# Kernel optimization log

Measured on AMD Instinct MI355X. Metric: run time of the kernel, lower is better.

Reference implementation:

```python
import jax, jax.numpy as jnp
import numpy as np
from jax import lax

IN_F = 512   # encoder output dim
MEL = 80     # mel bins (memory_dim)
R = 7        # reduction factor
ATT = 128    # attention dim
B = 64
T_ENC = 512
T_MEL = 700  # must be divisible by R -> 100 decoder steps


def _gru(x, h, w_ih, w_hh, b_ih, b_hh):
    # torch.nn.GRUCell math
    gi = x @ w_ih.T + b_ih
    gh = h @ w_hh.T + b_hh
    ir, iz, inn = jnp.split(gi, 3, axis=-1)
    hr, hz, hn = jnp.split(gh, 3, axis=-1)
    r = jax.nn.sigmoid(ir + hr)
    z = jax.nn.sigmoid(iz + hz)
    return (1.0 - z) * jnp.tanh(inn + r * hn) + z * h


_PARAM_SHAPES = {
    'prenet_w1': (256, MEL), 'prenet_b1': (256,),
    'prenet_w2': (128, 256), 'prenet_b2': (128,),
    'attrnn_w_ih': (768, IN_F + 128), 'attrnn_w_hh': (768, 256),
    'attrnn_b_ih': (768,), 'attrnn_b_hh': (768,),
    'q_w': (ATT, 256), 'inp_w': (ATT, IN_F), 'v_w': (1, ATT), 'v_b': (1,),
    'loc_conv': (32, 2, 31), 'loc_w': (ATT, 32),
    'pd_w': (256, 256 + IN_F), 'pd_b': (256,),
    'dec1_w_ih': (768, 256), 'dec1_w_hh': (768, 256), 'dec1_b_ih': (768,), 'dec1_b_hh': (768,),
    'dec2_w_ih': (768, 256), 'dec2_w_hh': (768, 256), 'dec2_b_ih': (768,), 'dec2_b_hh': (768,),
    'mel_w': (MEL * R, 256), 'mel_b': (MEL * R,),
    'stop_w': (1, 256 + MEL * R), 'stop_b': (1,),
}


def setup_inputs() -> dict:
    key = jax.random.key(0)
    ks = iter(jax.random.split(key, 40))
    d = {
        'inputs': jax.random.normal(next(ks), (B, T_ENC, IN_F), jnp.float32),
        'memory': jax.random.normal(next(ks), (B, T_MEL, MEL), jnp.float32),
        'mask': jnp.ones((B, T_ENC), dtype=bool),
    }
    for n, s in _PARAM_SHAPES.items():
        d[n] = jax.random.normal(next(ks), s, jnp.float32) * 0.02
    return d


def reference(inputs, memory, mask, prenet_w1, prenet_b1, prenet_w2, prenet_b2,
              attrnn_w_ih, attrnn_w_hh, attrnn_b_ih, attrnn_b_hh,
              q_w, inp_w, v_w, v_b, loc_conv, loc_w, pd_w, pd_b,
              dec1_w_ih, dec1_w_hh, dec1_b_ih, dec1_b_hh,
              dec2_w_ih, dec2_w_hh, dec2_b_ih, dec2_b_hh,
              mel_w, mel_b, stop_w, stop_b):
    Bq, T_enc, _ = inputs.shape
    # attention.preprocess_inputs: [B, T_enc, ATT], computed once
    proc_in = jnp.einsum('btd,ad->bta', inputs, inp_w)
    # _reshape_memory: [B, T_mel, MEL] -> [T_steps, B, R*MEL]
    mem = memory.reshape(Bq, -1, R * MEL).transpose(1, 0, 2)
    # teacher forcing: step 0 uses zero memory_input, step t uses frame t-1
    xs = jnp.concatenate([jnp.zeros_like(mem[:1]), mem[:-1]], axis=0)

    def step(carry, x):
        h_att, h1, h2, ctx, aw, awc = carry
        # memory_size<=0 path: keep last mel frame of previous group
        m_in = x[:, MEL * (R - 1):]
        # prenet (original, dropout disabled)
        p = jax.nn.relu(m_in @ prenet_w1.T + prenet_b1)
        p = jax.nn.relu(p @ prenet_w2.T + prenet_b2)
        # attention RNN
        h_att = _gru(jnp.concatenate([p, ctx], axis=-1), h_att,
                     attrnn_w_ih, attrnn_w_hh, attrnn_b_ih, attrnn_b_hh)
        # location-sensitive attention
        pq = h_att @ q_w.T                              # [B, ATT]
        loc = jnp.stack([aw, awc], axis=1)              # [B, 2, T_enc]
        pl = lax.conv_general_dilated(loc, loc_conv, (1,), [(15, 15)],
                                      dimension_numbers=('NCH', 'OIH', 'NCH'))
        pl = jnp.einsum('bct,ac->bta', pl, loc_w)       # [B, T_enc, ATT]
        e = (jnp.tanh(pq[:, None, :] + proc_in + pl) @ v_w.T)[..., 0] + v_b
        e = jnp.where(mask, e, -1e9)
        align = jax.nn.softmax(e, axis=-1)              # [B, T_enc]
        ctx = jnp.einsum('bt,btd->bd', align, inputs)   # [B, IN_F]
        awc = awc + align
        # decoder RNNs with residual connections
        dec = jnp.concatenate([h_att, ctx], axis=-1) @ pd_w.T + pd_b
        h1 = _gru(dec, h1, dec1_w_ih, dec1_w_hh, dec1_b_ih, dec1_b_hh)
        dec = h1 + dec
        h2 = _gru(dec, h2, dec2_w_ih, dec2_w_hh, dec2_b_ih, dec2_b_hh)
        dec = h2 + dec
        out = dec @ mel_w.T + mel_b                     # [B, R*MEL]
        # separate_stopnet=True: stopnet input is detached
        sin = lax.stop_gradient(jnp.concatenate([dec, out], axis=-1))
        stop = (sin @ stop_w.T + stop_b)[:, 0]
        return (h_att, h1, h2, ctx, align, awc), (out, align, stop)

    z = lambda n: jnp.zeros((Bq, n), inputs.dtype)
    zt = jnp.zeros((Bq, T_enc), inputs.dtype)
    carry0 = (z(256), z(256), z(256), z(IN_F), zt, zt)
    _, (outs, atts, stops) = lax.scan(step, carry0, xs)
    # _parse_outputs
    outputs = outs.transpose(1, 0, 2).reshape(Bq, -1, MEL).transpose(0, 2, 1)  # [B, MEL, T_mel]
    return outputs, atts.transpose(1, 0, 2), stops.T
```

## Files before the change

kernel.cpp:

```cpp
#include <hip/hip_runtime.h>
#include <hip/hip_bf16.h>


typedef unsigned int u32;

#ifndef __has_builtin
#define __has_builtin(x) 0
#endif

#define NSTEP 100

#define PK_ATTIH 0
#define PK_ATTHH 245760
#define PK_Q     344064
#define PK_PD    360448
#define PK_D1IH  458752
#define PK_D1HH  557056
#define PK_D2IH  655360
#define PK_D2HH  753664
#define PK_MEL   851968
#define W1T_U    923648
#define W2T_U    944128
#define PROCF_U  976896
#define P2ALL_U  3074048
#define INPT_U   3893248
#define MSTG_U   3958784
#define INF16_U  7542784
#define WS_NEED_U 15931392

#define OUT_ATT  3584000
#define OUT_STOP 6860800

typedef _Float16 h2 __attribute__((ext_vector_type(2)));
typedef float f32x4 __attribute__((ext_vector_type(4)));
typedef unsigned int u32x4 __attribute__((ext_vector_type(4)));
union U4 { uint4 v; _Float16 h[8]; };

__device__ __forceinline__ float fastrcp(float x) { return __builtin_amdgcn_rcpf(x); }
__device__ __forceinline__ float sig_p(float x) { return 1.f / (1.f + __expf(-x)); }
__device__ __forceinline__ float tanh_f(float x) {
    x = fminf(fmaxf(x, -15.f), 15.f);
    float e2 = __expf(2.f * x);
    return (e2 - 1.f) * fastrcp(e2 + 1.f);
}

__device__ __forceinline__ float dot2(u32 w, u32 x, float acc) {
    h2 wh = __builtin_bit_cast(h2, w);
    h2 xh = __builtin_bit_cast(h2, x);
#if __has_builtin(__builtin_amdgcn_fdot2)
    return __builtin_amdgcn_fdot2(wh, xh, acc, false);
#else
    return acc + (float)wh.x * (float)xh.x + (float)wh.y * (float)xh.y;
#endif
}

__device__ __forceinline__ u32 packh2(float a, float b) {
    h2 h; h.x = (_Float16)a; h.y = (_Float16)b;
    return __builtin_bit_cast(u32, h);
}

__device__ __forceinline__ float4 ntload_f4(const float* p) {
    f32x4 v = __builtin_nontemporal_load((const f32x4*)p);
    float4 r; r.x = v.x; r.y = v.y; r.z = v.z; r.w = v.w; return r;
}
__device__ __forceinline__ uint4 ntload_u4(const uint4* p) {
    u32x4 v = __builtin_nontemporal_load((const u32x4*)p);
    uint4 r; r.x = v.x; r.y = v.y; r.z = v.z; r.w = v.w; return r;
}
__device__ __forceinline__ float ntload_f(const float* p) {
    return __builtin_nontemporal_load(p);
}

__global__ void tkern(const float* __restrict__ src, float* __restrict__ dst, int O, int K) {
    int i = blockIdx.x * blockDim.x + threadIdx.x;
    if (i < O * K) {
        int o = i % O, k = i / O;
        dst[i] = src[o * K + k];
    }
}

__global__ void packw(const float* __restrict__ src, u32* __restrict__ dst, int O, int K) {
    int i = blockIdx.x * blockDim.x + threadIdx.x;
    int n = O * (K >> 1);
    if (i < n) {
        int o = i % O, p = i / O;
        dst[i] = packh2(src[o * K + 2 * p], src[o * K + 2 * p + 1]);
    }
}

__global__ void packi(const float* __restrict__ src, u32* __restrict__ dst) {
    int i = blockIdx.x * blockDim.x + threadIdx.x;
    if (i < 8388608) dst[i] = packh2(src[2 * i], src[2 * i + 1]);
}

__global__ void unmel(const float* __restrict__ ms, float* __restrict__ out) {
    int i = blockIdx.x * blockDim.x + threadIdx.x;
    if (i < 3584000) {
        int b = i / 56000, r = i % 56000;
        int mm = r / 700, c = r % 700;
        int step = c / 7, jj = c % 7;
        out[i] = ms[((size_t)b * 100 + step) * 560 + jj * 80 + mm];
    }
}

__global__ void prenet_kern(const float* __restrict__ memory,
                            const float* __restrict__ w1T, const float* __restrict__ b1,
                            const float* __restrict__ w2T, const float* __restrict__ b2,
                            float* __restrict__ p2all) {
    __shared__ float mi[80];
    __shared__ float p1[256];
    int blk = blockIdx.x;
    int t = blk >> 6, b = blk & 63;
    int tid = threadIdx.x;
    if (tid < 80) mi[tid] = (t == 0) ? 0.f : memory[(b * 700 + (7 * t - 1)) * 80 + tid];
    __syncthreads();
    float acc = b1[tid];
#pragma unroll 4
    for (int k = 0; k < 80; k++) acc += mi[k] * w1T[k * 256 + tid];
    p1[tid] = fmaxf(acc, 0.f);
    __syncthreads();
    if (tid < 128) {
        float a2 = b2[tid];
#pragma unroll 4
        for (int k = 0; k < 256; k++) a2 += p1[k] * w2T[k * 128 + tid];
        p2all[(t * 64 + b) * 128 + tid] = fmaxf(a2, 0.f);
    }
}

__global__ void proc_kern(const float* __restrict__ inputs, const float* __restrict__ inpT,
                          _Float16* __restrict__ procF) {
    __shared__ float xin[8][512];
    int blk = blockIdx.x;
    int b = blk >> 6, t0 = (blk & 63) << 3;
    int tid = threadIdx.x;
    for (int i = tid; i < 8 * 512; i += 1024)
        xin[i >> 9][i & 511] = inputs[((size_t)b * 512 + t0 + (i >> 9)) * 512 + (i & 511)];
    __syncthreads();
    int r = tid >> 7, a = tid & 127;
    float acc = 0.f;
#pragma unroll 4
    for (int d = 0; d < 512; d++) acc += xin[r][d] * inpT[d * 128 + a];
    procF[((size_t)(b * 512) + t0 + r) * 128 + a] = (_Float16)acc;
}

__launch_bounds__(1024, 1)
__global__ void decoder_kern(const float* __restrict__ inputs,
                             const u32* __restrict__ wsu,
                             const float* __restrict__ att_b_ih, const float* __restrict__ att_b_hh,
                             const float* __restrict__ v_w, const float* __restrict__ v_b,
                             const float* __restrict__ lcg, const float* __restrict__ lwg,
                             const float* __restrict__ pd_b,
                             const float* __restrict__ d1b_ih, const float* __restrict__ d1b_hh,
                             const float* __restrict__ d2b_ih, const float* __restrict__ d2b_hh,
                             const float* __restrict__ mel_b,
                             const float* __restrict__ stop_w, const float* __restrict__ stop_b,
                             float* __restrict__ out, int big) {
    const int b = blockIdx.x;
    const int tid = threadIdx.x;

    const uint4* w_attih = (const uint4*)(wsu + PK_ATTIH);
    const uint4* w_atthh = (const uint4*)(wsu + PK_ATTHH);
    const uint4* w_pd    = (const uint4*)(wsu + PK_PD);
    const uint4* w_d1ih  = (const uint4*)(wsu + PK_D1IH);
    const uint4* w_d1hh  = (const uint4*)(wsu + PK_D1HH);
    const uint4* w_d2ih  = (const uint4*)(wsu + PK_D2IH);
    const uint4* w_d2hh  = (const uint4*)(wsu + PK_D2HH);
    const uint4* w_mel   = (const uint4*)(wsu + PK_MEL);
    const _Float16* procF = (const _Float16*)(wsu + PROCF_U);
    const float* p2all   = (const float*)(wsu + P2ALL_U);
    const _Float16* inF16 = (const _Float16*)(wsu + INF16_U);
    float* mstage        = (float*)(wsu + MSTG_U);

    __shared__ float h_att[256], h1[256], h2[256], dec[256];
    __shared__ float awp[542], awcp[542];
    __shared__ __align__(16) float pqv[256];
    __shared__ float ebuf[512], red[32], mout[560];
    __shared__ __align__(16) u32 cbuf[16 * 513];
    __shared__ __align__(16) float scrA[4096];
    __shared__ __align__(16) float scrB[3072];
    __shared__ u32 xpatt[320];
    __shared__ u32 xppd[384];
    __shared__ u32 decp[128], h1p[128], h2p[128];
    __shared__ __align__(16) u32 lwp_lds[128 * 16];
    __shared__ __align__(16) float lcgT[62 * 32];
    __shared__ float bias[5424];
    __shared__ float stopws[816];

    for (int i = tid; i < 256; i += 1024) { h_att[i] = 0.f; h1[i] = 0.f; h2[i] = 0.f; dec[i] = 0.f; }
    for (int i = tid; i < 542; i += 1024) { awp[i] = 0.f; awcp[i] = 0.f; }
    for (int i = tid; i < 320; i += 1024) xpatt[i] = 0u;
    for (int i = tid; i < 384; i += 1024) xppd[i] = 0u;
    if (tid < 128) { decp[tid] = 0u; h1p[tid] = 0u; h2p[tid] = 0u; }
    for (int i = tid; i < 2048; i += 1024)
        lwp_lds[i] = packh2(lwg[2 * i], lwg[2 * i + 1]);
    for (int i = tid; i < 62 * 32; i += 1024) {
        int k = i >> 5, c = i & 31;
        lcgT[i] = lcg[c * 62 + k];
    }
    if (tid < 768) {
        bias[tid] = att_b_ih[tid]; bias[768 + tid] = att_b_hh[tid];
        bias[1536 + tid] = d1b_ih[tid]; bias[2304 + tid] = d1b_hh[tid];
        bias[3072 + tid] = d2b_ih[tid]; bias[3840 + tid] = d2b_hh[tid];
    }
    if (tid < 256) bias[4608 + tid] = pd_b[tid];
    if (tid < 560) bias[4864 + tid] = mel_b[tid];
    if (tid < 816) stopws[tid] = stop_w[tid];
    if (tid < 128) { pqv[2 * tid] = 0.f; pqv[2 * tid + 1] = v_w[tid]; }
    if (tid >= 960) {
        int j = tid - 960;
        xpatt[j] = packh2(p2all[(size_t)b * 128 + 2 * j], p2all[(size_t)b * 128 + 2 * j + 1]);
    }
    const float vb0 = v_b[0];
    const float sb0 = stop_b[0];
    __syncthreads();

    for (int step = 0; step < NSTEP; step++) {
        if (tid < 768) {
            const int og = tid % 192;
            const int ks = tid / 192;
            float4 ai = {0.f, 0.f, 0.f, 0.f};
            float4 ah4 = {0.f, 0.f, 0.f, 0.f};
#pragma unroll 8
            for (int p = ks * 80; p < ks * 80 + 80; p++) {
                uint4 w = w_attih[p * 192 + og];
                u32 x = xpatt[p];
                ai.x = dot2(w.x, x, ai.x); ai.y = dot2(w.y, x, ai.y);
                ai.z = dot2(w.z, x, ai.z); ai.w = dot2(w.w, x, ai.w);
            }
#pragma unroll 8
            for (int p = ks * 32; p < ks * 32 + 32; p++) {
                uint4 w = w_atthh[p * 192 + og];
                u32 x = xppd[p];
                ah4.x = dot2(w.x, x, ah4.x); ah4.y = dot2(w.y, x, ah4.y);
                ah4.z = dot2(w.z, x, ah4.z); ah4.w = dot2(w.w, x, ah4.w);
            }
            *(float4*)&scrA[ks * 768 + og * 4] = ai;
            *(float4*)&scrB[ks * 768 + og * 4] = ah4;
        }
        __syncthreads();

        if (tid < 128) {
            float hv[2];
#pragma unroll
            for (int j = 0; j < 2; j++) {
                const int o = tid * 2 + j;
                float gr = bias[o], gz = bias[256 + o], gn = bias[512 + o];
                float hr = bias[768 + o], hz = bias[1024 + o], hn = bias[1280 + o];
#pragma unroll
                for (int s = 0; s < 4; s++) {
                    gr += scrA[s * 768 + o]; gz += scrA[s * 768 + 256 + o]; gn += scrA[s * 768 + 512 + o];
                    hr += scrB[s * 768 + o]; hz += scrB[s * 768 + 256 + o]; hn += scrB[s * 768 + 512 + o];
                }
                float r = sig_p(gr + hr), z = sig_p(gz + hz);
                float n = tanh_f(gn + r * hn);
                hv[j] = (1.f - z) * n + z * h_att[o];
                h_att[o] = hv[j];
            }
            xppd[tid] = packh2(hv[0], hv[1]);
        }
        __syncthreads();

        if (tid < 128) {
            const u32* wqu = wsu + PK_Q;
            float qa = 0.f;
#pragma unroll 8
            for (int p = 0; p < 128; p++) qa = dot2(wqu[p * 128 + tid], xppd[p], qa);
            pqv[2 * tid] = qa;
        } else if (tid >= 512) {
            const int tp = tid - 512;
            float cr[32];
#pragma unroll
            for (int c = 0; c < 32; c++) cr[c] = 0.f;
#pragma clang loop unroll_count(2)
            for (int k = 0; k < 31; k++) {
                float a1 = awp[tp + k], a2 = awcp[tp + k];
                const float4* l1 = (const float4*)&lcgT[k * 32];
                const float4* l2 = (const float4*)&lcgT[(31 + k) * 32];
#pragma unroll
                for (int cc = 0; cc < 8; cc++) {
                    float4 w1 = l1[cc], w2 = l2[cc];
                    cr[4 * cc]     += w1.x * a1 + w2.x * a2;
                    cr[4 * cc + 1] += w1.y * a1 + w2.y * a2;
                    cr[4 * cc + 2] += w1.z * a1 + w2.z * a2;
                    cr[4 * cc + 3] += w1.w * a1 + w2.w * a2;
                }
            }
#pragma unroll
            for (int cp = 0; cp < 16; cp++) cbuf[cp * 513 + tp] = packh2(cr[2 * cp], cr[2 * cp + 1]);
        }
        __syncthreads();

        {
            const int wv = tid >> 6, lane = tid & 63;
            const int tg = wv & 3, ag = wv >> 2;
            const int a0 = ag << 5;
            const int t0 = (tg << 7) + lane;
            u32 crA[16], crB[16];
#pragma unroll
            for (int cp = 0; cp < 16; cp++) {
                crA[cp] = cbuf[cp * 513 + t0];
                crB[cp] = cbuf[cp * 513 + t0 + 64];
            }
            const uint4* pfA = (const uint4*)(procF + ((size_t)(b * 512 + t0)) * 128 + a0);
            const uint4* pfB = (const uint4*)(procF + ((size_t)(b * 512 + t0 + 64)) * 128 + a0);
            float acc0 = 0.f, acc1 = 0.f;
#pragma unroll
            for (int l = 0; l < 4; l++) {
                U4 uA; uA.v = ntload_u4(pfA + l);
                U4 uB; uB.v = ntload_u4(pfB + l);
#pragma unroll
                for (int j = 0; j < 8; j++) {
                    const int a = a0 + l * 8 + j;
                    float2 pv = *(const float2*)&pqv[2 * a];
                    const uint4* lw = (const uint4*)&lwp_lds[a * 16];
                    uint4 w0 = lw[0], w1 = lw[1], w2 = lw[2], w3 = lw[3];
                    float s0 = pv.x + (float)uA.h[j];
                    float s1 = pv.x + (float)uB.h[j];
                    s0 = dot2(w0.x, crA[0], s0);  s1 = dot2(w0.x, crB[0], s1);
                    s0 = dot2(w0.y, crA[1], s0);  s1 = dot2(w0.y, crB[1], s1);
                    s0 = dot2(w0.z, crA[2], s0);  s1 = dot2(w0.z, crB[2], s1);
                    s0 = dot2(w0.w, crA[3], s0);  s1 = dot2(w0.w, crB[3], s1);
                    s0 = dot2(w1.x, crA[4], s0);  s1 = dot2(w1.x, crB[4], s1);
                    s0 = dot2(w1.y, crA[5], s0);  s1 = dot2(w1.y, crB[5], s1);
                    s0 = dot2(w1.z, crA[6], s0);  s1 = dot2(w1.z, crB[6], s1);
                    s0 = dot2(w1.w, crA[7], s0);  s1 = dot2(w1.w, crB[7], s1);
                    s0 = dot2(w2.x, crA[8], s0);  s1 = dot2(w2.x, crB[8], s1);
                    s0 = dot2(w2.y, crA[9], s0);  s1 = dot2(w2.y, crB[9], s1);
                    s0 = dot2(w2.z, crA[10], s0); s1 = dot2(w2.z, crB[10], s1);
                    s0 = dot2(w2.w, crA[11], s0); s1 = dot2(w2.w, crB[11], s1);
                    s0 = dot2(w3.x, crA[12], s0); s1 = dot2(w3.x, crB[12], s1);
                    s0 = dot2(w3.y, crA[13], s0); s1 = dot2(w3.y, crB[13], s1);
                    s0 = dot2(w3.z, crA[14], s0); s1 = dot2(w3.z, crB[14], s1);
                    s0 = dot2(w3.w, crA[15], s0); s1 = dot2(w3.w, crB[15], s1);
                    acc0 += pv.y * tanh_f(s0);
                    acc1 += pv.y * tanh_f(s1);
                }
            }
            scrB[ag * 512 + t0] = acc0;
            scrB[ag * 512 + t0 + 64] = acc1;
        }
        __syncthreads();

        float e_reg = -1e30f;
        if (tid < 512)
            e_reg = scrB[tid] + scrB[512 + tid] + scrB[1024 + tid] + scrB[1536 + tid] + vb0;
        {
            float v = e_reg;
#pragma unroll
            for (int off = 32; off; off >>= 1) v = fmaxf(v, __shfl_down(v, off, 64));
            if (tid < 512 && (tid & 63) == 0) red[tid >> 6] = v;
        }
        __syncthreads();
        float smax = fmaxf(fmaxf(fmaxf(red[0], red[1]), fmaxf(red[2], red[3])),
                           fmaxf(fmaxf(red[4], red[5]), fmaxf(red[6], red[7])));
        float ex = 0.f;
        if (tid < 512) ex = __expf(e_reg - smax);
        {
            float v = ex;
#pragma unroll
            for (int off = 32; off; off >>= 1) v += __shfl_down(v, off, 64);
            if (tid < 512 && (tid & 63) == 0) red[8 + (tid >> 6)] = v;
        }
        __syncthreads();
        if (tid < 512) {
            float ssum = ((red[8] + red[9]) + (red[10] + red[11])) +
                         ((red[12] + red[13]) + (red[14] + red[15]));
            float al = ex * fastrcp(ssum);
            ebuf[tid] = al;
            awp[15 + tid] = al;
            awcp[15 + tid] += al;
            out[OUT_ATT + ((size_t)b * 100 + step) * 512 + tid] = al;
        }
        __syncthreads();

        if (big) {
            const int dg = tid & 63, ts = tid >> 6;
            const uint4* ib = (const uint4*)(inF16 + ((size_t)b * 512 + ts * 32) * 512 + dg * 8);
            float4 p0 = {0.f, 0.f, 0.f, 0.f}, p1 = {0.f, 0.f, 0.f, 0.f};
#pragma unroll 8
            for (int t = 0; t < 32; t++) {
                float al = ebuf[ts * 32 + t];
                U4 u; u.v = ntload_u4(ib + (size_t)t * 64);
                p0.x += al * (float)u.h[0]; p0.y += al * (float)u.h[1];
                p0.z += al * (float)u.h[2]; p0.w += al * (float)u.h[3];
                p1.x += al * (float)u.h[4]; p1.y += al * (float)u.h[5];
                p1.z += al * (float)u.h[6]; p1.w += al * (float)u.h[7];
            }
            float* scrF = (float*)cbuf;
            *(float4*)&scrF[ts * 512 + dg * 8] = p0;
            *(float4*)&scrF[ts * 512 + dg * 8 + 4] = p1;
        } else {
            const int dg = tid & 127, ts = tid >> 7;
            const float* ib = inputs + ((size_t)b * 512 + ts * 64) * 512;
            float4 acc = {0.f, 0.f, 0.f, 0.f};
#pragma unroll 8
            for (int t = 0; t < 64; t++) {
                float al = ebuf[ts * 64 + t];
                float4 xv = ntload_f4(ib + (size_t)t * 512 + dg * 4);
                acc.x += al * xv.x; acc.y += al * xv.y; acc.z += al * xv.z; acc.w += al * xv.w;
            }
            *(float4*)&scrA[ts * 512 + dg * 4] = acc;
        }
        __syncthreads();

        if (tid < 256) {
            float s0 = 0.f, s1 = 0.f;
            if (big) {
                const float* scrF = (const float*)cbuf;
#pragma unroll
                for (int q = 0; q < 16; q++) { s0 += scrF[q * 512 + 2 * tid]; s1 += scrF[q * 512 + 2 * tid + 1]; }
            } else {
#pragma unroll
                for (int q = 0; q < 8; q++) { s0 += scrA[q * 512 + 2 * tid]; s1 += scrA[q * 512 + 2 * tid + 1]; }
            }
            u32 pr = packh2(s0, s1);
            xpatt[64 + tid] = pr;
            xppd[128 + tid] = pr;
        }
        __syncthreads();

        {
            const int og = tid & 63, ks = tid >> 6;
            float4 acc = {0.f, 0.f, 0.f, 0.f};
#pragma unroll 8
            for (int p = ks * 24; p < ks * 24 + 24; p++) {
                uint4 w = w_pd[p * 64 + og];
                u32 x = xppd[p];
                acc.x = dot2(w.x, x, acc.x); acc.y = dot2(w.y, x, acc.y);
                acc.z = dot2(w.z, x, acc.z); acc.w = dot2(w.w, x, acc.w);
            }
            *(float4*)&scrA[ks * 256 + og * 4] = acc;
        }
        __syncthreads();

        if (tid < 128) {
            float d0 = bias[4608 + 2 * tid], d1 = bias[4608 + 2 * tid + 1];
#pragma unroll
            for (int q = 0; q < 16; q++) { d0 += scrA[q * 256 + 2 * tid]; d1 += scrA[q * 256 + 2 * tid + 1]; }
            dec[2 * tid] = d0; dec[2 * tid + 1] = d1;
            decp[tid] = packh2(d0, d1);
        }
        __syncthreads();

        if (tid < 768) {
            const int og = tid % 192;
            const int ks = tid / 192;
            float4 ai = {0.f, 0.f, 0.f, 0.f};
            float4 ah4 = {0.f, 0.f, 0.f, 0.f};
#pragma unroll 8
            for (int p = ks * 32; p < ks * 32 + 32; p++) {
                uint4 w1 = w_d1ih[p * 192 + og];
                uint4 w2 = w_d1hh[p * 192 + og];
                u32 xd = decp[p], xh = h1p[p];
                ai.x = dot2(w1.x, xd, ai.x); ai.y = dot2(w1.y, xd, ai.y);
                ai.z = dot2(w1.z, xd, ai.z); ai.w = dot2(w1.w, xd, ai.w);
                ah4.x = dot2(w2.x, xh, ah4.x); ah4.y = dot2(w2.y, xh, ah4.y);
                ah4.z = dot2(w2.z, xh, ah4.z); ah4.w = dot2(w2.w, xh, ah4.w);
            }
            *(float4*)&scrA[ks * 768 + og * 4] = ai;
            *(float4*)&scrB[ks * 768 + og * 4] = ah4;
        }
        __syncthreads();

        if (tid < 128) {
            float hv[2], dv[2];
#pragma unroll
            for (int j = 0; j < 2; j++) {
                const int o = tid * 2 + j;
                float gr = bias[1536 + o], gz = bias[1792 + o], gn = bias[2048 + o];
                float hr = bias[2304 + o], hz = bias[2560 + o], hn = bias[2816 + o];
#pragma unroll
                for (int s = 0; s < 4; s++) {
                    gr += scrA[s * 768 + o]; gz += scrA[s * 768 + 256 + o]; gn += scrA[s * 768 + 512 + o];
                    hr += scrB[s * 768 + o]; hz += scrB[s * 768 + 256 + o]; hn += scrB[s * 768 + 512 + o];
                }
                float r = sig_p(gr + hr), z = sig_p(gz + hz);
                float n = tanh_f(gn + r * hn);
                hv[j] = (1.f - z) * n + z * h1[o];
                h1[o] = hv[j];
                dv[j] = hv[j] + dec[o];
                dec[o] = dv[j];
            }
            h1p[tid] = packh2(hv[0], hv[1]);
            decp[tid] = packh2(dv[0], dv[1]);
        }
        __syncthreads();

        if (tid < 768) {
            const int og = tid % 192;
            const int ks = tid / 192;
            float4 ai = {0.f, 0.f, 0.f, 0.f};
            float4 ah4 = {0.f, 0.f, 0.f, 0.f};
#pragma unroll 8
            for (int p = ks * 32; p < ks * 32 + 32; p++) {
                uint4 w1 = w_d2ih[p * 192 + og];
                uint4 w2 = w_d2hh[p * 192 + og];
                u32 xd = decp[p], xh = h2p[p];
                ai.x = dot2(w1.x, xd, ai.x); ai.y = dot2(w1.y, xd, ai.y);
                ai.z = dot2(w1.z, xd, ai.z); ai.w = dot2(w1.w, xd, ai.w);
                ah4.x = dot2(w2.x, xh, ah4.x); ah4.y = dot2(w2.y, xh, ah4.y);
                ah4.z = dot2(w2.z, xh, ah4.z); ah4.w = dot2(w2.w, xh, ah4.w);
            }
            *(float4*)&scrA[ks * 768 + og * 4] = ai;
            *(float4*)&scrB[ks * 768 + og * 4] = ah4;
        }
        __syncthreads();

        if (tid < 128) {
            float hv[2], dv[2];
#pragma unroll
            for (int j = 0; j < 2; j++) {
                const int o = tid * 2 + j;
                float gr = bias[3072 + o], gz = bias[3328 + o], gn = bias[3584 + o];
                float hr = bias[3840 + o], hz = bias[4096 + o], hn = bias[4352 + o];
#pragma unroll
                for (int s = 0; s < 4; s++) {
                    gr += scrA[s * 768 + o]; gz += scrA[s * 768 + 256 + o]; gn += scrA[s * 768 + 512 + o];
                    hr += scrB[s * 768 + o]; hz += scrB[s * 768 + 256 + o]; hn += scrB[s * 768 + 512 + o];
                }
                float r = sig_p(gr + hr), z = sig_p(gz + hz);
                float n = tanh_f(gn + r * hn);
                hv[j] = (1.f - z) * n + z * h2[o];
                h2[o] = hv[j];
                dv[j] = hv[j] + dec[o];
                dec[o] = dv[j];
            }
            h2p[tid] = packh2(hv[0], hv[1]);
            decp[tid] = packh2(dv[0], dv[1]);
        }
        __syncthreads();

        if (tid < 560) {
            const int og = tid % 140;
            const int ks = tid / 140;
            float4 acc = {0.f, 0.f, 0.f, 0.f};
#pragma unroll 8
            for (int p = ks * 32; p < ks * 32 + 32; p++) {
                uint4 w = w_mel[p * 140 + og];
                u32 x = decp[p];
                acc.x = dot2(w.x, x, acc.x); acc.y = dot2(w.y, x, acc.y);
                acc.z = dot2(w.z, x, acc.z); acc.w = dot2(w.w, x, acc.w);
            }
            *(float4*)&scrA[ks * 560 + og * 4] = acc;
        }
        __syncthreads();

        if (tid < 280) {
#pragma unroll
            for (int j = 0; j < 2; j++) {
                const int o = 2 * tid + j;
                float m = bias[4864 + o];
#pragma unroll
                for (int s = 0; s < 4; s++) m += scrA[s * 560 + o];
                mout[o] = m;
                if (big) {
                    mstage[((size_t)b * 100 + step) * 560 + o] = m;
                } else {
                    int mm = o % 80, jj = o / 80;
                    out[((size_t)b * 80 + mm) * 700 + 7 * step + jj] = m;
                }
            }
        }
        __syncthreads();

        {
            float v = 0.f;
            if (tid < 816) v = ((tid < 256) ? dec[tid] : mout[tid - 256]) * stopws[tid];
            if (tid < 832) {
#pragma unroll
                for (int off = 32; off; off >>= 1) v += __shfl_down(v, off, 64);
                if ((tid & 63) == 0) red[tid >> 6] = v;
            }
            if (tid >= 960 && step + 1 < NSTEP) {
                int j = tid - 960;
                const float* p2n = p2all + ((size_t)(step + 1) * 64 + b) * 128;
                xpatt[j] = packh2(ntload_f(p2n + 2 * j), ntload_f(p2n + 2 * j + 1));
            }
        }
        __syncthreads();
        if (tid == 0) {
            float s = sb0;
            for (int w = 0; w < 13; w++) s += red[w];
            out[OUT_STOP + (size_t)b * 100 + step] = s;
        }
    }
}

extern "C" void kernel_launch(void* const* d_in, const int* in_sizes, int n_in,
                              void* d_out, int out_size, void* d_ws, size_t ws_size,
                              hipStream_t stream) {
    const float* inputs    = (const float*)d_in[0];
    const float* memory    = (const float*)d_in[1];
    const float* prenet_w1 = (const float*)d_in[3];
    const float* prenet_b1 = (const float*)d_in[4];
    const float* prenet_w2 = (const float*)d_in[5];
    const float* prenet_b2 = (const float*)d_in[6];
    const float* att_w_ih  = (const float*)d_in[7];
    const float* att_w_hh  = (const float*)d_in[8];
    const float* att_b_ih  = (const float*)d_in[9];
    const float* att_b_hh  = (const float*)d_in[10];
    const float* q_w       = (const float*)d_in[11];
    const float* inp_w     = (const float*)d_in[12];
    const float* v_w       = (const float*)d_in[13];
    const float* v_b       = (const float*)d_in[14];
    const float* loc_conv  = (const float*)d_in[15];
    const float* loc_w     = (const float*)d_in[16];
    const float* pd_w      = (const float*)d_in[17];
    const float* pd_b      = (const float*)d_in[18];
    const float* d1_w_ih   = (const float*)d_in[19];
    const float* d1_w_hh   = (const float*)d_in[20];
    const float* d1_b_ih   = (const float*)d_in[21];
    const float* d1_b_hh   = (const float*)d_in[22];
    const float* d2_w_ih   = (const float*)d_in[23];
    const float* d2_w_hh   = (const float*)d_in[24];
    const float* d2_b_ih   = (const float*)d_in[25];
    const float* d2_b_hh   = (const float*)d_in[26];
    const float* mel_w     = (const float*)d_in[27];
    const float* mel_b     = (const float*)d_in[28];
    const float* stop_w    = (const float*)d_in[29];
    const float* stop_b    = (const float*)d_in[30];

    u32* wsu = (u32*)d_ws;
    float* out = (float*)d_out;
    const int big = ws_size >= (size_t)WS_NEED_U * 4u;

    auto P = [&](const float* src, int off, int O, int K) {
        int n = O * (K / 2);
        packw<<<(n + 255) / 256, 256, 0, stream>>>(src, wsu + off, O, K);
    };
    P(att_w_ih, PK_ATTIH, 768, 640);
    P(att_w_hh, PK_ATTHH, 768, 256);
    P(q_w,      PK_Q,     128, 256);
    P(pd_w,     PK_PD,    256, 768);
    P(d1_w_ih,  PK_D1IH,  768, 256);
    P(d1_w_hh,  PK_D1HH,  768, 256);
    P(d2_w_ih,  PK_D2IH,  768, 256);
    P(d2_w_hh,  PK_D2HH,  768, 256);
    P(mel_w,    PK_MEL,   560, 256);

    tkern<<<(256 * 80 + 255) / 256, 256, 0, stream>>>(prenet_w1, (float*)(wsu + W1T_U), 256, 80);
    tkern<<<(128 * 256 + 255) / 256, 256, 0, stream>>>(prenet_w2, (float*)(wsu + W2T_U), 128, 256);

    prenet_kern<<<6400, 256, 0, stream>>>(memory, (float*)(wsu + W1T_U), prenet_b1,
                                          (float*)(wsu + W2T_U), prenet_b2,
                                          (float*)(wsu + P2ALL_U));

    {
        float* inpT = (float*)(wsu + INPT_U);
        tkern<<<(128 * 512 + 255) / 256, 256, 0, stream>>>(inp_w, inpT, 128, 512);
        proc_kern<<<4096, 1024, 0, stream>>>(inputs, inpT, (_Float16*)(wsu + PROCF_U));
    }

    if (big) packi<<<32768, 256, 0, stream>>>(inputs, wsu + INF16_U);

    decoder_kern<<<64, 1024, 0, stream>>>(inputs, wsu,
                                          att_b_ih, att_b_hh, v_w, v_b,
                                          loc_conv, loc_w, pd_b,
                                          d1_b_ih, d1_b_hh, d2_b_ih, d2_b_hh,
                                          mel_b, stop_w, stop_b, out, big);

    if (big) unmel<<<14000, 256, 0, stream>>>((const float*)(wsu + MSTG_U), out);
}
```

Measured before the change: 15.09 ms.

## Process two batch rows per decoder block to reuse weight loads

The persistent decoder kernel now handles two batch elements per workgroup (32 blocks instead of 64), so each fp16 weight fetched from global memory in the GRU, projection and mel matvecs is applied to two input vectors. Shared buffers are doubled, the location conv weights and biases are read from global memory or a pre-transposed workspace instead of LDS, and softmax and stop reductions are done per batch half. This halves weight traffic per step but uses only half as many CUs and gives each thread more serial work in the attention and conv phases.

```diff
diff --git a/kernel.cpp b/kernel.cpp
--- a/kernel.cpp
+++ b/kernel.cpp
@@ -70,6 +70,9 @@
 __device__ __forceinline__ float ntload_f(const float* p) {
     return __builtin_nontemporal_load(p);
 }
+__device__ __forceinline__ void ntstore_f(float* p, float v) {
+    __builtin_nontemporal_store(v, p);
+}
 
 __global__ void tkern(const float* __restrict__ src, float* __restrict__ dst, int O, int K) {
     int i = blockIdx.x * blockDim.x + threadIdx.x;
@@ -91,6 +94,11 @@
 __global__ void packi(const float* __restrict__ src, u32* __restrict__ dst) {
     int i = blockIdx.x * blockDim.x + threadIdx.x;
     if (i < 8388608) dst[i] = packh2(src[2 * i], src[2 * i + 1]);
+}
+
+__global__ void tlcg(const float* __restrict__ lcg, float* __restrict__ dst) {
+    int i = blockIdx.x * blockDim.x + threadIdx.x;
+    if (i < 1984) { int k = i >> 5, c = i & 31; dst[i] = lcg[c * 62 + k]; }
 }
 
 __global__ void unmel(const float* __restrict__ ms, float* __restrict__ out) {
@@ -148,14 +156,14 @@
                              const u32* __restrict__ wsu,
                              const float* __restrict__ att_b_ih, const float* __restrict__ att_b_hh,
                              const float* __restrict__ v_w, const float* __restrict__ v_b,
-                             const float* __restrict__ lcg, const float* __restrict__ lwg,
+                             const float* __restrict__ lcgTg, const float* __restrict__ lwg,
                              const float* __restrict__ pd_b,
                              const float* __restrict__ d1b_ih, const float* __restrict__ d1b_hh,
                              const float* __restrict__ d2b_ih, const float* __restrict__ d2b_hh,
                              const float* __restrict__ mel_b,
                              const float* __restrict__ stop_w, const float* __restrict__ stop_b,
                              float* __restrict__ out, int big) {
-    const int b = blockIdx.x;
+    const int blk = blockIdx.x;
     const int tid = threadIdx.x;
 
     const uint4* w_attih = (const uint4*)(wsu + PK_ATTIH);
@@ -171,44 +179,33 @@
     const _Float16* inF16 = (const _Float16*)(wsu + INF16_U);
     float* mstage        = (float*)(wsu + MSTG_U);
 
-    __shared__ float h_att[256], h1[256], h2[256], dec[256];
-    __shared__ float awp[542], awcp[542];
-    __shared__ __align__(16) float pqv[256];
-    __shared__ float ebuf[512], red[32], mout[560];
-    __shared__ __align__(16) u32 cbuf[16 * 513];
+    __shared__ float h_att[512], h1[512], h2[512], dec[512];
+    __shared__ float awp[1084], awcp[1084];
+    __shared__ __align__(16) float pqv[512];
+    __shared__ float red[32], mout[1120];
+    __shared__ __align__(16) u32 cbuf[2 * 16 * 513];
     __shared__ __align__(16) float scrA[4096];
-    __shared__ __align__(16) float scrB[3072];
-    __shared__ u32 xpatt[320];
-    __shared__ u32 xppd[384];
-    __shared__ u32 decp[128], h1p[128], h2p[128];
+    __shared__ __align__(16) float scrB[4096];
+    __shared__ u32 xpatt[640];
+    __shared__ u32 xppd[768];
+    __shared__ u32 decp[256], h1p[256], h2p[256];
     __shared__ __align__(16) u32 lwp_lds[128 * 16];
-    __shared__ __align__(16) float lcgT[62 * 32];
-    __shared__ float bias[5424];
-    __shared__ float stopws[816];
-
-    for (int i = tid; i < 256; i += 1024) { h_att[i] = 0.f; h1[i] = 0.f; h2[i] = 0.f; dec[i] = 0.f; }
-    for (int i = tid; i < 542; i += 1024) { awp[i] = 0.f; awcp[i] = 0.f; }
-    for (int i = tid; i < 320; i += 1024) xpatt[i] = 0u;
-    for (int i = tid; i < 384; i += 1024) xppd[i] = 0u;
-    if (tid < 128) { decp[tid] = 0u; h1p[tid] = 0u; h2p[tid] = 0u; }
+
+    float* scrH = (float*)cbuf;
+
+    for (int i = tid; i < 512; i += 1024) { h_att[i] = 0.f; h1[i] = 0.f; h2[i] = 0.f; dec[i] = 0.f; }
+    for (int i = tid; i < 1084; i += 1024) { awp[i] = 0.f; awcp[i] = 0.f; }
+    for (int i = tid; i < 640; i += 1024) xpatt[i] = 0u;
+    for (int i = tid; i < 768; i += 1024) xppd[i] = 0u;
+    if (tid < 256) { decp[tid] = 0u; h1p[tid] = 0u; h2p[tid] = 0u; }
     for (int i = tid; i < 2048; i += 1024)
         lwp_lds[i] = packh2(lwg[2 * i], lwg[2 * i + 1]);
-    for (int i = tid; i < 62 * 32; i += 1024) {
-        int k = i >> 5, c = i & 31;
-        lcgT[i] = lcg[c * 62 + k];
-    }
-    if (tid < 768) {
-        bias[tid] = att_b_ih[tid]; bias[768 + tid] = att_b_hh[tid];
-        bias[1536 + tid] = d1b_ih[tid]; bias[2304 + tid] = d1b_hh[tid];
-        bias[3072 + tid] = d2b_ih[tid]; bias[3840 + tid] = d2b_hh[tid];
-    }
-    if (tid < 256) bias[4608 + tid] = pd_b[tid];
-    if (tid < 560) bias[4864 + tid] = mel_b[tid];
-    if (tid < 816) stopws[tid] = stop_w[tid];
-    if (tid < 128) { pqv[2 * tid] = 0.f; pqv[2 * tid + 1] = v_w[tid]; }
+    if (tid < 256) { pqv[2 * tid] = 0.f; pqv[2 * tid + 1] = v_w[tid & 127]; }
     if (tid >= 960) {
         int j = tid - 960;
-        xpatt[j] = packh2(p2all[(size_t)b * 128 + 2 * j], p2all[(size_t)b * 128 + 2 * j + 1]);
+        const float* p20 = p2all + (size_t)(blk * 2) * 128;
+        xpatt[j]       = packh2(p20[2 * j], p20[2 * j + 1]);
+        xpatt[320 + j] = packh2(p20[128 + 2 * j], p20[128 + 2 * j + 1]);
     }
     const float vb0 = v_b[0];
     const float sb0 = stop_b[0];
@@ -218,100 +215,118 @@
         if (tid < 768) {
             const int og = tid % 192;
             const int ks = tid / 192;
-            float4 ai = {0.f, 0.f, 0.f, 0.f};
-            float4 ah4 = {0.f, 0.f, 0.f, 0.f};
+            float4 ai0 = {0.f,0.f,0.f,0.f}, ai1 = {0.f,0.f,0.f,0.f};
+            float4 ah0 = {0.f,0.f,0.f,0.f}, ah1 = {0.f,0.f,0.f,0.f};
 #pragma unroll 8
             for (int p = ks * 80; p < ks * 80 + 80; p++) {
                 uint4 w = w_attih[p * 192 + og];
-                u32 x = xpatt[p];
-                ai.x = dot2(w.x, x, ai.x); ai.y = dot2(w.y, x, ai.y);
-                ai.z = dot2(w.z, x, ai.z); ai.w = dot2(w.w, x, ai.w);
+                u32 x0 = xpatt[p], x1 = xpatt[320 + p];
+                ai0.x = dot2(w.x, x0, ai0.x); ai0.y = dot2(w.y, x0, ai0.y);
+                ai0.z = dot2(w.z, x0, ai0.z); ai0.w = dot2(w.w, x0, ai0.w);
+                ai1.x = dot2(w.x, x1, ai1.x); ai1.y = dot2(w.y, x1, ai1.y);
+                ai1.z = dot2(w.z, x1, ai1.z); ai1.w = dot2(w.w, x1, ai1.w);
             }
 #pragma unroll 8
             for (int p = ks * 32; p < ks * 32 + 32; p++) {
                 uint4 w = w_atthh[p * 192 + og];
-                u32 x = xppd[p];
-                ah4.x = dot2(w.x, x, ah4.x); ah4.y = dot2(w.y, x, ah4.y);
-                ah4.z = dot2(w.z, x, ah4.z); ah4.w = dot2(w.w, x, ah4.w);
-            }
-            *(float4*)&scrA[ks * 768 + og * 4] = ai;
-            *(float4*)&scrB[ks * 768 + og * 4] = ah4;
-        }
-        __syncthreads();
-
-        if (tid < 128) {
+                u32 x0 = xppd[p], x1 = xppd[384 + p];
+                ah0.x = dot2(w.x, x0, ah0.x); ah0.y = dot2(w.y, x0, ah0.y);
+                ah0.z = dot2(w.z, x0, ah0.z); ah0.w = dot2(w.w, x0, ah0.w);
+                ah1.x = dot2(w.x, x1, ah1.x); ah1.y = dot2(w.y, x1, ah1.y);
+                ah1.z = dot2(w.z, x1, ah1.z); ah1.w = dot2(w.w, x1, ah1.w);
+            }
+            *(float4*)&scrA[ks * 768 + og * 4] = ai0;
+            *(float4*)&scrB[ks * 768 + og * 4] = ai1;
+            *(float4*)&scrH[ks * 768 + og * 4] = ah0;
+            *(float4*)&scrH[3072 + ks * 768 + og * 4] = ah1;
+        }
+        __syncthreads();
+
+        if (tid < 256) {
+            const int bt = tid >> 7, lo = tid & 127;
+            const float* P = bt ? scrB : scrA;
+            const float* H = scrH + bt * 3072;
             float hv[2];
 #pragma unroll
             for (int j = 0; j < 2; j++) {
-                const int o = tid * 2 + j;
-                float gr = bias[o], gz = bias[256 + o], gn = bias[512 + o];
-                float hr = bias[768 + o], hz = bias[1024 + o], hn = bias[1280 + o];
+                const int o = lo * 2 + j;
+                float gr = att_b_ih[o], gz = att_b_ih[256 + o], gn = att_b_ih[512 + o];
+                float hr = att_b_hh[o], hz = att_b_hh[256 + o], hn = att_b_hh[512 + o];
 #pragma unroll
                 for (int s = 0; s < 4; s++) {
-                    gr += scrA[s * 768 + o]; gz += scrA[s * 768 + 256 + o]; gn += scrA[s * 768 + 512 + o];
-                    hr += scrB[s * 768 + o]; hz += scrB[s * 768 + 256 + o]; hn += scrB[s * 768 + 512 + o];
+                    gr += P[s * 768 + o]; gz += P[s * 768 + 256 + o]; gn += P[s * 768 + 512 + o];
+                    hr += H[s * 768 + o]; hz += H[s * 768 + 256 + o]; hn += H[s * 768 + 512 + o];
                 }
                 float r = sig_p(gr + hr), z = sig_p(gz + hz);
                 float n = tanh_f(gn + r * hn);
-                hv[j] = (1.f - z) * n + z * h_att[o];
-                h_att[o] = hv[j];
-            }
-            xppd[tid] = packh2(hv[0], hv[1]);
-        }
-        __syncthreads();
-
-        if (tid < 128) {
+                hv[j] = (1.f - z) * n + z * h_att[bt * 256 + o];
+                h_att[bt * 256 + o] = hv[j];
+            }
+            xppd[bt * 384 + lo] = packh2(hv[0], hv[1]);
+        }
+        __syncthreads();
+
+        if (tid < 256) {
+            const int bt = tid >> 7, a = tid & 127;
             const u32* wqu = wsu + PK_Q;
+            const u32* xp = xppd + bt * 384;
             float qa = 0.f;
 #pragma unroll 8
-            for (int p = 0; p < 128; p++) qa = dot2(wqu[p * 128 + tid], xppd[p], qa);
-            pqv[2 * tid] = qa;
-        } else if (tid >= 512) {
-            const int tp = tid - 512;
-            float cr[32];
-#pragma unroll
-            for (int c = 0; c < 32; c++) cr[c] = 0.f;
+            for (int p = 0; p < 128; p++) qa = dot2(wqu[p * 128 + a], xp[p], qa);
+            pqv[bt * 256 + 2 * a] = qa;
+        } else {
+            auto conv_one = [&](int idx) {
+                const int bt = idx >> 9, tp = idx & 511;
+                float cr[32];
+#pragma unroll
+                for (int c = 0; c < 32; c++) cr[c] = 0.f;
 #pragma clang loop unroll_count(2)
-            for (int k = 0; k < 31; k++) {
-                float a1 = awp[tp + k], a2 = awcp[tp + k];
-                const float4* l1 = (const float4*)&lcgT[k * 32];
-                const float4* l2 = (const float4*)&lcgT[(31 + k) * 32];
-#pragma unroll
-                for (int cc = 0; cc < 8; cc++) {
-                    float4 w1 = l1[cc], w2 = l2[cc];
-                    cr[4 * cc]     += w1.x * a1 + w2.x * a2;
-                    cr[4 * cc + 1] += w1.y * a1 + w2.y * a2;
-                    cr[4 * cc + 2] += w1.z * a1 + w2.z * a2;
-                    cr[4 * cc + 3] += w1.w * a1 + w2.w * a2;
-                }
-            }
-#pragma unroll
-            for (int cp = 0; cp < 16; cp++) cbuf[cp * 513 + tp] = packh2(cr[2 * cp], cr[2 * cp + 1]);
+                for (int k = 0; k < 31; k++) {
+                    float a1 = awp[bt * 542 + tp + k], a2 = awcp[bt * 542 + tp + k];
+                    const float4* l1 = (const float4*)&lcgTg[k * 32];
+                    const float4* l2 = (const float4*)&lcgTg[(31 + k) * 32];
+#pragma unroll
+                    for (int cc = 0; cc < 8; cc++) {
+                        float4 w1 = l1[cc], w2 = l2[cc];
+                        cr[4 * cc]     += w1.x * a1 + w2.x * a2;
+                        cr[4 * cc + 1] += w1.y * a1 + w2.y * a2;
+                        cr[4 * cc + 2] += w1.z * a1 + w2.z * a2;
+                        cr[4 * cc + 3] += w1.w * a1 + w2.w * a2;
+                    }
+                }
+#pragma unroll
+                for (int cp = 0; cp < 16; cp++)
+                    cbuf[bt * 8208 + cp * 513 + tp] = packh2(cr[2 * cp], cr[2 * cp + 1]);
+            };
+            const int j = tid - 256;
+            conv_one(j);
+            if (j < 256) conv_one(j + 768);
         }
         __syncthreads();
 
         {
             const int wv = tid >> 6, lane = tid & 63;
-            const int tg = wv & 3, ag = wv >> 2;
-            const int a0 = ag << 5;
+            const int bt = wv >> 3, w8 = wv & 7;
+            const int tg = w8 & 3, ag = w8 >> 2;
+            const int a0 = ag << 6;
             const int t0 = (tg << 7) + lane;
             u32 crA[16], crB[16];
 #pragma unroll
             for (int cp = 0; cp < 16; cp++) {
-                crA[cp] = cbuf[cp * 513 + t0];
-                crB[cp] = cbuf[cp * 513 + t0 + 64];
-            }
-            const uint4* pfA = (const uint4*)(procF + ((size_t)(b * 512 + t0)) * 128 + a0);
-            const uint4* pfB = (const uint4*)(procF + ((size_t)(b * 512 + t0 + 64)) * 128 + a0);
+                crA[cp] = cbuf[bt * 8208 + cp * 513 + t0];
+                crB[cp] = cbuf[bt * 8208 + cp * 513 + t0 + 64];
+            }
+            const uint4* pfA = (const uint4*)(procF + ((size_t)((blk * 2 + bt) * 512 + t0)) * 128 + a0);
+            const uint4* pfB = (const uint4*)(procF + ((size_t)((blk * 2 + bt) * 512 + t0 + 64)) * 128 + a0);
             float acc0 = 0.f, acc1 = 0.f;
 #pragma unroll
-            for (int l = 0; l < 4; l++) {
+            for (int l = 0; l < 8; l++) {
                 U4 uA; uA.v = ntload_u4(pfA + l);
                 U4 uB; uB.v = ntload_u4(pfB + l);
 #pragma unroll
                 for (int j = 0; j < 8; j++) {
                     const int a = a0 + l * 8 + j;
-                    float2 pv = *(const float2*)&pqv[2 * a];
+                    float2 pv = *(const float2*)&pqv[bt * 256 + 2 * a];
                     const uint4* lw = (const uint4*)&lwp_lds[a * 16];
                     uint4 w0 = lw[0], w1 = lw[1], w2 = lw[2], w3 = lw[3];
                     float s0 = pv.x + (float)uA.h[j];
@@ -336,252 +351,291 @@
                     acc1 += pv.y * tanh_f(s1);
                 }
             }
-            scrB[ag * 512 + t0] = acc0;
-            scrB[ag * 512 + t0 + 64] = acc1;
-        }
-        __syncthreads();
-
-        float e_reg = -1e30f;
-        if (tid < 512)
-            e_reg = scrB[tid] + scrB[512 + tid] + scrB[1024 + tid] + scrB[1536 + tid] + vb0;
+            scrA[bt * 1024 + ag * 512 + t0] = acc0;
+            scrA[bt * 1024 + ag * 512 + t0 + 64] = acc1;
+        }
+        __syncthreads();
+
         {
+            const int bt = tid >> 9, t = tid & 511;
+            float e_reg = scrA[bt * 1024 + t] + scrA[bt * 1024 + 512 + t] + vb0;
             float v = e_reg;
 #pragma unroll
             for (int off = 32; off; off >>= 1) v = fmaxf(v, __shfl_down(v, off, 64));
-            if (tid < 512 && (tid & 63) == 0) red[tid >> 6] = v;
-        }
-        __syncthreads();
-        float smax = fmaxf(fmaxf(fmaxf(red[0], red[1]), fmaxf(red[2], red[3])),
-                           fmaxf(fmaxf(red[4], red[5]), fmaxf(red[6], red[7])));
-        float ex = 0.f;
-        if (tid < 512) ex = __expf(e_reg - smax);
+            if ((tid & 63) == 0) red[tid >> 6] = v;
+            __syncthreads();
+            float smax = fmaxf(fmaxf(fmaxf(red[bt*8+0], red[bt*8+1]), fmaxf(red[bt*8+2], red[bt*8+3])),
+                               fmaxf(fmaxf(red[bt*8+4], red[bt*8+5]), fmaxf(red[bt*8+6], red[bt*8+7])));
+            float ex = __expf(e_reg - smax);
+            v = ex;
+#pragma unroll
+            for (int off = 32; off; off >>= 1) v += __shfl_down(v, off, 64);
+            if ((tid & 63) == 0) red[16 + (tid >> 6)] = v;
+            __syncthreads();
+            float ssum = ((red[16+bt*8+0] + red[16+bt*8+1]) + (red[16+bt*8+2] + red[16+bt*8+3])) +
+                         ((red[16+bt*8+4] + red[16+bt*8+5]) + (red[16+bt*8+6] + red[16+bt*8+7]));
+            float al = ex * fastrcp(ssum);
+            awp[bt * 542 + 15 + t] = al;
+            awcp[bt * 542 + 15 + t] += al;
+            ntstore_f(&out[OUT_ATT + ((size_t)(blk * 2 + bt) * 100 + step) * 512 + t], al);
+        }
+        __syncthreads();
+
         {
-            float v = ex;
-#pragma unroll
-            for (int off = 32; off; off >>= 1) v += __shfl_down(v, off, 64);
-            if (tid < 512 && (tid & 63) == 0) red[8 + (tid >> 6)] = v;
-        }
-        __syncthreads();
+            float* scrF = (float*)cbuf;
+            const int bt = tid >> 9, r = tid & 511;
+            if (big) {
+                const int dg = r & 63, ts = r >> 6;
+                const uint4* ib = (const uint4*)(inF16 + ((size_t)((blk * 2 + bt) * 512) + ts * 64) * 512 + dg * 8);
+                const float* alp = &awp[bt * 542 + 15 + ts * 64];
+                float4 p0 = {0.f,0.f,0.f,0.f}, p1 = {0.f,0.f,0.f,0.f};
+#pragma unroll 8
+                for (int t = 0; t < 64; t++) {
+                    float al = alp[t];
+                    U4 u; u.v = ntload_u4(ib + (size_t)t * 64);
+                    p0.x += al * (float)u.h[0]; p0.y += al * (float)u.h[1];
+                    p0.z += al * (float)u.h[2]; p0.w += al * (float)u.h[3];
+                    p1.x += al * (float)u.h[4]; p1.y += al * (float)u.h[5];
+                    p1.z += al * (float)u.h[6]; p1.w += al * (float)u.h[7];
+                }
+                *(float4*)&scrF[bt * 4096 + ts * 512 + dg * 8] = p0;
+                *(float4*)&scrF[bt * 4096 + ts * 512 + dg * 8 + 4] = p1;
+            } else {
+                const int dg = r & 127, ts = r >> 7;
+                const float* ib = inputs + ((size_t)((blk * 2 + bt) * 512) + ts * 128) * 512;
+                const float* alp = &awp[bt * 542 + 15 + ts * 128];
+                float4 acc = {0.f,0.f,0.f,0.f};
+#pragma unroll 8
+                for (int t = 0; t < 128; t++) {
+                    float al = alp[t];
+                    float4 xv = ntload_f4(ib + (size_t)t * 512 + dg * 4);
+                    acc.x += al * xv.x; acc.y += al * xv.y; acc.z += al * xv.z; acc.w += al * xv.w;
+                }
+                *(float4*)&scrF[bt * 4096 + ts * 512 + dg * 4] = acc;
+            }
+        }
+        __syncthreads();
+
         if (tid < 512) {
-            float ssum = ((red[8] + red[9]) + (red[10] + red[11])) +
-                         ((red[12] + red[13]) + (red[14] + red[15]));
-            float al = ex * fastrcp(ssum);
-            ebuf[tid] = al;
-            awp[15 + tid] = al;
-            awcp[15 + tid] += al;
-            out[OUT_ATT + ((size_t)b * 100 + step) * 512 + tid] = al;
-        }
-        __syncthreads();
-
-        if (big) {
-            const int dg = tid & 63, ts = tid >> 6;
-            const uint4* ib = (const uint4*)(inF16 + ((size_t)b * 512 + ts * 32) * 512 + dg * 8);
-            float4 p0 = {0.f, 0.f, 0.f, 0.f}, p1 = {0.f, 0.f, 0.f, 0.f};
-#pragma unroll 8
-            for (int t = 0; t < 32; t++) {
-                float al = ebuf[ts * 32 + t];
-                U4 u; u.v = ntload_u4(ib + (size_t)t * 64);
-                p0.x += al * (float)u.h[0]; p0.y += al * (float)u.h[1];
-                p0.z += al * (float)u.h[2]; p0.w += al * (float)u.h[3];
-                p1.x += al * (float)u.h[4]; p1.y += al * (float)u.h[5];
-                p1.z += al * (float)u.h[6]; p1.w += al * (float)u.h[7];
-            }
-            float* scrF = (float*)cbuf;
-            *(float4*)&scrF[ts * 512 + dg * 8] = p0;
-            *(float4*)&scrF[ts * 512 + dg * 8 + 4] = p1;
-        } else {
-            const int dg = tid & 127, ts = tid >> 7;
-            const float* ib = inputs + ((size_t)b * 512 + ts * 64) * 512;
-            float4 acc = {0.f, 0.f, 0.f, 0.f};
-#pragma unroll 8
-            for (int t = 0; t < 64; t++) {
-                float al = ebuf[ts * 64 + t];
-                float4 xv = ntload_f4(ib + (size_t)t * 512 + dg * 4);
-                acc.x += al * xv.x; acc.y += al * xv.y; acc.z += al * xv.z; acc.w += al * xv.w;
-            }
-            *(float4*)&scrA[ts * 512 + dg * 4] = acc;
-        }
-        __syncthreads();
-
-        if (tid < 256) {
+            const int bt = tid >> 8, lo = tid & 255;
+            const float* scrF = (const float*)cbuf;
             float s0 = 0.f, s1 = 0.f;
             if (big) {
-                const float* scrF = (const float*)cbuf;
-#pragma unroll
-                for (int q = 0; q < 16; q++) { s0 += scrF[q * 512 + 2 * tid]; s1 += scrF[q * 512 + 2 * tid + 1]; }
+#pragma unroll
+                for (int q = 0; q < 8; q++) { s0 += scrF[bt*4096 + q*512 + 2*lo]; s1 += scrF[bt*4096 + q*512 + 2*lo + 1]; }
             } else {
 #pragma unroll
-                for (int q = 0; q < 8; q++) { s0 += scrA[q * 512 + 2 * tid]; s1 += scrA[q * 512 + 2 * tid + 1]; }
+                for (int q = 0; q < 4; q++) { s0 += scrF[bt*4096 + q*512 + 2*lo]; s1 += scrF[bt*4096 + q*512 + 2*lo + 1]; }
             }
             u32 pr = packh2(s0, s1);
-            xpatt[64 + tid] = pr;
-            xppd[128 + tid] = pr;
+            xpatt[bt * 320 + 64 + lo] = pr;
+            xppd[bt * 384 + 128 + lo] = pr;
         }
         __syncthreads();
 
         {
             const int og = tid & 63, ks = tid >> 6;
-            float4 acc = {0.f, 0.f, 0.f, 0.f};
+            float4 a0 = {0.f,0.f,0.f,0.f}, a1 = {0.f,0.f,0.f,0.f};
 #pragma unroll 8
             for (int p = ks * 24; p < ks * 24 + 24; p++) {
                 uint4 w = w_pd[p * 64 + og];
-                u32 x = xppd[p];
-                acc.x = dot2(w.x, x, acc.x); acc.y = dot2(w.y, x, acc.y);
-                acc.z = dot2(w.z, x, acc.z); acc.w = dot2(w.w, x, acc.w);
-            }
-            *(float4*)&scrA[ks * 256 + og * 4] = acc;
-        }
-        __syncthreads();
-
-        if (tid < 128) {
-            float d0 = bias[4608 + 2 * tid], d1 = bias[4608 + 2 * tid + 1];
-#pragma unroll
-            for (int q = 0; q < 16; q++) { d0 += scrA[q * 256 + 2 * tid]; d1 += scrA[q * 256 + 2 * tid + 1]; }
-            dec[2 * tid] = d0; dec[2 * tid + 1] = d1;
-            decp[tid] = packh2(d0, d1);
+                u32 x0 = xppd[p], x1 = xppd[384 + p];
+                a0.x = dot2(w.x, x0, a0.x); a0.y = dot2(w.y, x0, a0.y);
+                a0.z = dot2(w.z, x0, a0.z); a0.w = dot2(w.w, x0, a0.w);
+                a1.x = dot2(w.x, x1, a1.x); a1.y = dot2(w.y, x1, a1.y);
+                a1.z = dot2(w.z, x1, a1.z); a1.w = dot2(w.w, x1, a1.w);
+            }
+            *(float4*)&scrA[ks * 256 + og * 4] = a0;
+            *(float4*)&scrB[ks * 256 + og * 4] = a1;
+        }
+        __syncthreads();
+
+        if (tid < 256) {
+            const int bt = tid >> 7, lo = tid & 127;
+            const float* P = bt ? scrB : scrA;
+            float d0 = pd_b[2 * lo], d1 = pd_b[2 * lo + 1];
+#pragma unroll
+            for (int q = 0; q < 16; q++) { d0 += P[q * 256 + 2 * lo]; d1 += P[q * 256 + 2 * lo + 1]; }
+            dec[bt * 256 + 2 * lo] = d0; dec[bt * 256 + 2 * lo + 1] = d1;
+            decp[bt * 128 + lo] = packh2(d0, d1);
         }
         __syncthreads();
 
         if (tid < 768) {
             const int og = tid % 192;
             const int ks = tid / 192;
-            float4 ai = {0.f, 0.f, 0.f, 0.f};
-            float4 ah4 = {0.f, 0.f, 0.f, 0.f};
+            float4 ai0 = {0.f,0.f,0.f,0.f}, ai1 = {0.f,0.f,0.f,0.f};
+            float4 ah0 = {0.f,0.f,0.f,0.f}, ah1 = {0.f,0.f,0.f,0.f};
 #pragma unroll 8
             for (int p = ks * 32; p < ks * 32 + 32; p++) {
                 uint4 w1 = w_d1ih[p * 192 + og];
                 uint4 w2 = w_d1hh[p * 192 + og];
-                u32 xd = decp[p], xh = h1p[p];
-                ai.x = dot2(w1.x, xd, ai.x); ai.y = dot2(w1.y, xd, ai.y);
-                ai.z = dot2(w1.z, xd, ai.z); ai.w = dot2(w1.w, xd, ai.w);
-                ah4.x = dot2(w2.x, xh, ah4.x); ah4.y = dot2(w2.y, xh, ah4.y);
-                ah4.z = dot2(w2.z, xh, ah4.z); ah4.w = dot2(w2.w, xh, ah4.w);
-            }
-            *(float4*)&scrA[ks * 768 + og * 4] = ai;
-            *(float4*)&scrB[ks * 768 + og * 4] = ah4;
-        }
-        __syncthreads();
-
-        if (tid < 128) {
+                u32 xd0 = decp[p], xd1 = decp[128 + p];
+                u32 xh0 = h1p[p],  xh1 = h1p[128 + p];
+                ai0.x = dot2(w1.x, xd0, ai0.x); ai0.y = dot2(w1.y, xd0, ai0.y);
+                ai0.z = dot2(w1.z, xd0, ai0.z); ai0.w = dot2(w1.w, xd0, ai0.w);
+                ai1.x = dot2(w1.x, xd1, ai1.x); ai1.y = dot2(w1.y, xd1, ai1.y);
+                ai1.z = dot2(w1.z, xd1, ai1.z); ai1.w = dot2(w1.w, xd1, ai1.w);
+                ah0.x = dot2(w2.x, xh0, ah0.x); ah0.y = dot2(w2.y, xh0, ah0.y);
+                ah0.z = dot2(w2.z, xh0, ah0.z); ah0.w = dot2(w2.w, xh0, ah0.w);
+                ah1.x = dot2(w2.x, xh1, ah1.x); ah1.y = dot2(w2.y, xh1, ah1.y);
+                ah1.z = dot2(w2.z, xh1, ah1.z); ah1.w = dot2(w2.w, xh1, ah1.w);
+            }
+            *(float4*)&scrA[ks * 768 + og * 4] = ai0;
+            *(float4*)&scrB[ks * 768 + og * 4] = ai1;
+            *(float4*)&scrH[ks * 768 + og * 4] = ah0;
+            *(float4*)&scrH[3072 + ks * 768 + og * 4] = ah1;
+        }
+        __syncthreads();
+
+        if (tid < 256) {
+            const int bt = tid >> 7, lo = tid & 127;
+            const float* P = bt ? scrB : scrA;
+            const float* H = scrH + bt * 3072;
             float hv[2], dv[2];
 #pragma unroll
             for (int j = 0; j < 2; j++) {
-                const int o = tid * 2 + j;
-                float gr = bias[1536 + o], gz = bias[1792 + o], gn = bias[2048 + o];
-                float hr = bias[2304 + o], hz = bias[2560 + o], hn = bias[2816 + o];
+                const int o = lo * 2 + j;
+                float gr = d1b_ih[o], gz = d1b_ih[256 + o], gn = d1b_ih[512 + o];
+                float hr = d1b_hh[o], hz = d1b_hh[256 + o], hn = d1b_hh[512 + o];
 #pragma unroll
                 for (int s = 0; s < 4; s++) {
-                    gr += scrA[s * 768 + o]; gz += scrA[s * 768 + 256 + o]; gn += scrA[s * 768 + 512 + o];
-                    hr += scrB[s * 768 + o]; hz += scrB[s * 768 + 256 + o]; hn += scrB[s * 768 + 512 + o];
+                    gr += P[s * 768 + o]; gz += P[s * 768 + 256 + o]; gn += P[s * 768 + 512 + o];
+                    hr += H[s * 768 + o]; hz += H[s * 768 + 256 + o]; hn += H[s * 768 + 512 + o];
                 }
                 float r = sig_p(gr + hr), z = sig_p(gz + hz);
                 float n = tanh_f(gn + r * hn);
-                hv[j] = (1.f - z) * n + z * h1[o];
-                h1[o] = hv[j];
-                dv[j] = hv[j] + dec[o];
-                dec[o] = dv[j];
-            }
-            h1p[tid] = packh2(hv[0], hv[1]);
-            decp[tid] = packh2(dv[0], dv[1]);
+                hv[j] = (1.f - z) * n + z * h1[bt * 256 + o];
+                h1[bt * 256 + o] = hv[j];
+                dv[j] = hv[j] + dec[bt * 256 + o];
+                dec[bt * 256 + o] = dv[j];
+            }
+            h1p[bt * 128 + lo] = packh2(hv[0], hv[1]);
+            decp[bt * 128 + lo] = packh2(dv[0], dv[1]);
         }
         __syncthreads();
 
         if (tid < 768) {
             const int og = tid % 192;
             const int ks = tid / 192;
-            float4 ai = {0.f, 0.f, 0.f, 0.f};
-            float4 ah4 = {0.f, 0.f, 0.f, 0.f};
+            float4 ai0 = {0.f,0.f,0.f,0.f}, ai1 = {0.f,0.f,0.f,0.f};
+            float4 ah0 = {0.f,0.f,0.f,0.f}, ah1 = {0.f,0.f,0.f,0.f};
 #pragma unroll 8
             for (int p = ks * 32; p < ks * 32 + 32; p++) {
                 uint4 w1 = w_d2ih[p * 192 + og];
                 uint4 w2 = w_d2hh[p * 192 + og];
-                u32 xd = decp[p], xh = h2p[p];
-                ai.x = dot2(w1.x, xd, ai.x); ai.y = dot2(w1.y, xd, ai.y);
-                ai.z = dot2(w1.z, xd, ai.z); ai.w = dot2(w1.w, xd, ai.w);
-                ah4.x = dot2(w2.x, xh, ah4.x); ah4.y = dot2(w2.y, xh, ah4.y);
-                ah4.z = dot2(w2.z, xh, ah4.z); ah4.w = dot2(w2.w, xh, ah4.w);
-            }
-            *(float4*)&scrA[ks * 768 + og * 4] = ai;
-            *(float4*)&scrB[ks * 768 + og * 4] = ah4;
-        }
-        __syncthreads();
-
-        if (tid < 128) {
+                u32 xd0 = decp[p], xd1 = decp[128 + p];
+                u32 xh0 = h2p[p],  xh1 = h2p[128 + p];
+                ai0.x = dot2(w1.x, xd0, ai0.x); ai0.y = dot2(w1.y, xd0, ai0.y);
+                ai0.z = dot2(w1.z, xd0, ai0.z); ai0.w = dot2(w1.w, xd0, ai0.w);
+                ai1.x = dot2(w1.x, xd1, ai1.x); ai1.y = dot2(w1.y, xd1, ai1.y);
+                ai1.z = dot2(w1.z, xd1, ai1.z); ai1.w = dot2(w1.w, xd1, ai1.w);
+                ah0.x = dot2(w2.x, xh0, ah0.x); ah0.y = dot2(w2.y, xh0, ah0.y);
+                ah0.z = dot2(w2.z, xh0, ah0.z); ah0.w = dot2(w2.w, xh0, ah0.w);
+                ah1.x = dot2(w2.x, xh1, ah1.x); ah1.y = dot2(w2.y, xh1, ah1.y);
+                ah1.z = dot2(w2.z, xh1, ah1.z); ah1.w = dot2(w2.w, xh1, ah1.w);
+            }
+            *(float4*)&scrA[ks * 768 + og * 4] = ai0;
+            *(float4*)&scrB[ks * 768 + og * 4] = ai1;
+            *(float4*)&scrH[ks * 768 + og * 4] = ah0;
+            *(float4*)&scrH[3072 + ks * 768 + og * 4] = ah1;
+        }
+        __syncthreads();
+
+        if (tid < 256) {
+            const int bt = tid >> 7, lo = tid & 127;
+            const float* P = bt ? scrB : scrA;
+            const float* H = scrH + bt * 3072;
             float hv[2], dv[2];
 #pragma unroll
             for (int j = 0; j < 2; j++) {
-                const int o = tid * 2 + j;
-                float gr = bias[3072 + o], gz = bias[3328 + o], gn = bias[3584 + o];
-                float hr = bias[3840 + o], hz = bias[4096 + o], hn = bias[4352 + o];
+                const int o = lo * 2 + j;
+                float gr = d2b_ih[o], gz = d2b_ih[256 + o], gn = d2b_ih[512 + o];
+                float hr = d2b_hh[o], hz = d2b_hh[256 + o], hn = d2b_hh[512 + o];
 #pragma unroll
                 for (int s = 0; s < 4; s++) {
-                    gr += scrA[s * 768 + o]; gz += scrA[s * 768 + 256 + o]; gn += scrA[s * 768 + 512 + o];
-                    hr += scrB[s * 768 + o]; hz += scrB[s * 768 + 256 + o]; hn += scrB[s * 768 + 512 + o];
+                    gr += P[s * 768 + o]; gz += P[s * 768 + 256 + o]; gn += P[s * 768 + 512 + o];
+                    hr += H[s * 768 + o]; hz += H[s * 768 + 256 + o]; hn += H[s * 768 + 512 + o];
                 }
                 float r = sig_p(gr + hr), z = sig_p(gz + hz);
                 float n = tanh_f(gn + r * hn);
-                hv[j] = (1.f - z) * n + z * h2[o];
-                h2[o] = hv[j];
-                dv[j] = hv[j] + dec[o];
-                dec[o] = dv[j];
-            }
-            h2p[tid] = packh2(hv[0], hv[1]);
-            decp[tid] = packh2(dv[0], dv[1]);
+                hv[j] = (1.f - z) * n + z * h2[bt * 256 + o];
+                h2[bt * 256 + o] = hv[j];
+                dv[j] = hv[j] + dec[bt * 256 + o];
+                dec[bt * 256 + o] = dv[j];
+            }
+            h2p[bt * 128 + lo] = packh2(hv[0], hv[1]);
+            decp[bt * 128 + lo] = packh2(dv[0], dv[1]);
         }
         __syncthreads();
 
         if (tid < 560) {
             const int og = tid % 140;
             const int ks = tid / 140;
-            float4 acc = {0.f, 0.f, 0.f, 0.f};
+            float4 a0 = {0.f,0.f,0.f,0.f}, a1 = {0.f,0.f,0.f,0.f};
 #pragma unroll 8
             for (int p = ks * 32; p < ks * 32 + 32; p++) {
                 uint4 w = w_mel[p * 140 + og];
-                u32 x = decp[p];
-                acc.x = dot2(w.x, x, acc.x); acc.y = dot2(w.y, x, acc.y);
-                acc.z = dot2(w.z, x, acc.z); acc.w = dot2(w.w, x, acc.w);
-            }
-            *(float4*)&scrA[ks * 560 + og * 4] = acc;
-        }
-        __syncthreads();
-
-        if (tid < 280) {
+                u32 x0 = decp[p], x1 = decp[128 + p];
+                a0.x = dot2(w.x, x0, a0.x); a0.y = dot2(w.y, x0, a0.y);
+                a0.z = dot2(w.z, x0, a0.z); a0.w = dot2(w.w, x0, a0.w);
+                a1.x = dot2(w.x, x1, a1.x); a1.y = dot2(w.y, x1, a1.y);
+                a1.z = dot2(w.z, x1, a1.z); a1.w = dot2(w.w, x1, a1.w);
+            }
+            *(float4*)&scrA[ks * 560 + og * 4] = a0;
+            *(float4*)&scrB[ks * 560 + og * 4] = a1;
+        }
+        __syncthreads();
+
+        if (tid < 560) {
+            const int bt = (tid >= 280) ? 1 : 0;
+            const int lo = bt ? (tid - 280) : tid;
+            const float* P = bt ? scrB : scrA;
 #pragma unroll
             for (int j = 0; j < 2; j++) {
-                const int o = 2 * tid + j;
-                float m = bias[4864 + o];
-#pragma unroll
-                for (int s = 0; s < 4; s++) m += scrA[s * 560 + o];
-                mout[o] = m;
+                const int o = 2 * lo + j;
+                float m = mel_b[o];
+#pragma unroll
+                for (int s = 0; s < 4; s++) m += P[s * 560 + o];
+                mout[bt * 560 + o] = m;
                 if (big) {
-                    mstage[((size_t)b * 100 + step) * 560 + o] = m;
+                    mstage[((size_t)(blk * 2 + bt) * 100 + step) * 560 + o] = m;
                 } else {
                     int mm = o % 80, jj = o / 80;
-                    out[((size_t)b * 80 + mm) * 700 + 7 * step + jj] = m;
+                    out[((size_t)(blk * 2 + bt) * 80 + mm) * 700 + 7 * step + jj] = m;
                 }
             }
         }
         __syncthreads();
 
         {
-            float v = 0.f;
-            if (tid < 816) v = ((tid < 256) ? dec[tid] : mout[tid - 256]) * stopws[tid];
+            float v0 = 0.f, v1 = 0.f;
+            if (tid < 816) {
+                float w = stop_w[tid];
+                if (tid < 256) { v0 = dec[tid] * w; v1 = dec[256 + tid] * w; }
+                else { v0 = mout[tid - 256] * w; v1 = mout[560 + tid - 256] * w; }
+            }
             if (tid < 832) {
 #pragma unroll
-                for (int off = 32; off; off >>= 1) v += __shfl_down(v, off, 64);
-                if ((tid & 63) == 0) red[tid >> 6] = v;
+                for (int off = 32; off; off >>= 1) {
+                    v0 += __shfl_down(v0, off, 64);
+                    v1 += __shfl_down(v1, off, 64);
+                }
+                if ((tid & 63) == 0) { red[tid >> 6] = v0; red[16 + (tid >> 6)] = v1; }
             }
             if (tid >= 960 && step + 1 < NSTEP) {
                 int j = tid - 960;
-                const float* p2n = p2all + ((size_t)(step + 1) * 64 + b) * 128;
-                xpatt[j] = packh2(ntload_f(p2n + 2 * j), ntload_f(p2n + 2 * j + 1));
+                const float* p2n = p2all + ((size_t)(step + 1) * 64 + blk * 2) * 128;
+                xpatt[j]       = packh2(ntload_f(p2n + 2 * j), ntload_f(p2n + 2 * j + 1));
+                xpatt[320 + j] = packh2(ntload_f(p2n + 128 + 2 * j), ntload_f(p2n + 128 + 2 * j + 1));
             }
         }
         __syncthreads();
         if (tid == 0) {
-            float s = sb0;
-            for (int w = 0; w < 13; w++) s += red[w];
-            out[OUT_STOP + (size_t)b * 100 + step] = s;
+            float s0 = sb0, s1 = sb0;
+            for (int w = 0; w < 13; w++) { s0 += red[w]; s1 += red[16 + w]; }
+            ntstore_f(&out[OUT_STOP + (size_t)(blk * 2) * 100 + step], s0);
+            ntstore_f(&out[OUT_STOP + (size_t)(blk * 2 + 1) * 100 + step], s1);
         }
     }
 }
@@ -653,9 +707,11 @@
 
     if (big) packi<<<32768, 256, 0, stream>>>(inputs, wsu + INF16_U);
 
-    decoder_kern<<<64, 1024, 0, stream>>>(inputs, wsu,
+    tlcg<<<8, 256, 0, stream>>>(loc_conv, (float*)(wsu + INPT_U));
+
+    decoder_kern<<<32, 1024, 0, stream>>>(inputs, wsu,
                                           att_b_ih, att_b_hh, v_w, v_b,
-                                          loc_conv, loc_w, pd_b,
+                                          (const float*)(wsu + INPT_U), loc_w, pd_b,
                                           d1_b_ih, d1_b_hh, d2_b_ih, d2_b_hh,
                                           mel_b, stop_w, stop_b, out, big);
 
```

Measured after the change: 23.25 ms. +54.1%, slower.
